# Optimization experiments

Hardware: AMD Instinct MI355X
Metric: run time of the kernel (lower is better)

## Reference

```python
import jax, jax.numpy as jnp
import numpy as np

B, T, H = 4, 2048, 1024
NH, NKV, HD = 16, 4, 64  # heads, kv heads, head_dim

def setup_inputs() -> dict:
    key = jax.random.key(0)
    ks = jax.random.split(key, 5)
    s = 0.02
    return {
        "x": jax.random.normal(ks[0], (B, T, H), dtype=jnp.float32),
        "wq": jax.random.normal(ks[1], (H, NH * HD), dtype=jnp.float32) * s,
        "wk": jax.random.normal(ks[2], (H, NKV * HD), dtype=jnp.float32) * s,
        "wv": jax.random.normal(ks[3], (H, NKV * HD), dtype=jnp.float32) * s,
        "wo": jax.random.normal(ks[4], (NH * HD, H), dtype=jnp.float32) * s,
    }

def reference(x, wq, wk, wv, wo):
    b, t, _ = x.shape
    q = (x @ wq).reshape(b, t, NH, HD).transpose(0, 2, 1, 3)    # [B,NH,T,HD]
    k = (x @ wk).reshape(b, t, NKV, HD).transpose(0, 2, 1, 3)   # [B,NKV,T,HD]
    v = (x @ wv).reshape(b, t, NKV, HD).transpose(0, 2, 1, 3)
    n_rep = NH // NKV
    # repeat_kv: expand each kv head n_rep times along the head axis
    k_rep = jnp.repeat(k, n_rep, axis=1)                        # [B,NH,T,HD]
    v_rep = jnp.repeat(v, n_rep, axis=1)
    scale = 1.0 / np.sqrt(HD).astype(np.float32)
    scores = jnp.einsum('bhqd,bhkd->bhqk', q, k_rep) * scale    # [B,NH,T,T]
    key_pos = jnp.arange(t)[None, :]
    q_pos = jnp.arange(t)[:, None]  # past_len = 0 (no kv cache)
    causal = key_pos > q_pos                                    # [T,T]
    scores = jnp.where(causal[None, None], -jnp.inf, scores)
    probs = jax.nn.softmax(scores, axis=-1)                     # dropout is identity (eval / rate 0)
    attn = jnp.einsum('bhqk,bhkd->bhqd', probs, v_rep)          # [B,NH,T,HD]
    attn = attn.transpose(0, 2, 1, 3).reshape(b, t, NH * HD)
    return attn @ wo
```

## Files before the change

kernel.cpp:

```cpp
#include <hip/hip_runtime.h>
#include <hip/hip_bf16.h>

using bf16 = __hip_bfloat16;
typedef __attribute__((ext_vector_type(8))) short bf16x8;
typedef __attribute__((ext_vector_type(4))) short bf16x4;
typedef __attribute__((ext_vector_type(4))) float f32x4;

typedef const __attribute__((address_space(1))) void* as1_t;
typedef __attribute__((address_space(3))) void* as3_t;
__device__ __forceinline__ void load_lds16(const void* g, void* l) {
    __builtin_amdgcn_global_load_lds((as1_t)g, (as3_t)l, 16, 0, 0);
}

__global__ __launch_bounds__(256) void cast_f32_bf16(const float* __restrict__ src,
                                                     bf16* __restrict__ dst, int n4) {
    int i = (blockIdx.x * 256 + threadIdx.x);
    if (i >= n4) return;
    const float4 v = *(const float4*)(src + (long)i * 4);
    bf16 t[4];
    t[0] = __float2bfloat16(v.x);
    t[1] = __float2bfloat16(v.y);
    t[2] = __float2bfloat16(v.z);
    t[3] = __float2bfloat16(v.w);
    *(uint2*)(dst + (long)i * 4) = *(uint2*)t;
}

__global__ __launch_bounds__(256) void transpose_cast(const float* __restrict__ src,
                                                      int K, int N, bf16* __restrict__ dst) {
    __shared__ float tile[32][33];
    const int tx = threadIdx.x & 31;
    const int ty = threadIdx.x >> 5;
    const int n0 = blockIdx.x * 32;
    const int k0 = blockIdx.y * 32;
    for (int i = 0; i < 32; i += 8)
        tile[ty + i][tx] = src[(long)(k0 + ty + i) * N + n0 + tx];
    __syncthreads();
    for (int i = 0; i < 32; i += 8)
        dst[(long)(n0 + ty + i) * K + k0 + tx] = __float2bfloat16(tile[tx][ty + i]);
}

__global__ __launch_bounds__(256) void transpose_v(const bf16* __restrict__ qkv,
                                                   bf16* __restrict__ vt) {
    __shared__ bf16 tile[64][72];
    const int tb = blockIdx.x, kvh = blockIdx.y, b = blockIdx.z;
    const int r = threadIdx.x >> 3;
    const int c = (threadIdx.x & 7) * 8;
    const bf16* src = qkv + (long)(b * 2048 + tb * 64) * 1536 + 1280 + kvh * 64;
    *(uint4*)&tile[r][c]      = *(const uint4*)(src + (long)r * 1536 + c);
    *(uint4*)&tile[r + 32][c] = *(const uint4*)(src + (long)(r + 32) * 1536 + c);
    __syncthreads();
    bf16* dst = vt + (long)(b * 4 + kvh) * 64 * 2048 + tb * 64;
#pragma unroll
    for (int rr = 0; rr < 2; rr++) {
        const int d = r + rr * 32;
        bf16 t8[8];
#pragma unroll
        for (int e = 0; e < 8; e++) t8[e] = tile[c + e][d];
        *(uint4*)(dst + (long)d * 2048 + c) = *(uint4*)t8;
    }
}

template <bool BF16_OUT>
__global__ __launch_bounds__(256) void gemm_bt(const bf16* __restrict__ A,
                                               const bf16* __restrict__ Bt,
                                               void* __restrict__ C,
                                               int M, int N, int K) {
    __shared__ bf16 Ash[128 * 32];
    __shared__ bf16 Bsh[128 * 32];
    const int tid  = threadIdx.x;
    const int lane = tid & 63;
    const int wid  = tid >> 6;
    const int wm   = (wid >> 1) * 64;
    const int wn   = (wid & 1) * 64;
    const int quad = lane >> 4;
    const int l16  = lane & 15;
    const int bm = blockIdx.x, bn = blockIdx.y;

    const int r_l   = lane >> 2;
    const int cslot = lane & 3;
    const int cdat  = (cslot - (r_l >> 1)) & 3;

    const bf16* pa0 = A  + (long)(bm * 128 + wid * 32 + r_l) * K + cdat * 8;
    const bf16* pa1 = pa0 + (long)16 * K;
    const bf16* pb0 = Bt + (long)(bn * 128 + wid * 32 + r_l) * K + cdat * 8;
    const bf16* pb1 = pb0 + (long)16 * K;
    bf16* la0 = Ash + (wid * 32) * 32;
    bf16* la1 = Ash + (wid * 32 + 16) * 32;
    bf16* lb0 = Bsh + (wid * 32) * 32;
    bf16* lb1 = Bsh + (wid * 32 + 16) * 32;

    const int sw = ((quad + (l16 >> 1)) & 3) * 8;

    f32x4 acc[4][4] = {};

    for (int k0 = 0; k0 < K; k0 += 32) {
        __syncthreads();
        load_lds16(pa0 + k0, la0);
        load_lds16(pa1 + k0, la1);
        load_lds16(pb0 + k0, lb0);
        load_lds16(pb1 + k0, lb1);
        __syncthreads();

        bf16x8 af[4], bfr[4];
#pragma unroll
        for (int i = 0; i < 4; i++) af[i]  = *(const bf16x8*)&Ash[(wm + i * 16 + l16) * 32 + sw];
#pragma unroll
        for (int j = 0; j < 4; j++) bfr[j] = *(const bf16x8*)&Bsh[(wn + j * 16 + l16) * 32 + sw];
#pragma unroll
        for (int i = 0; i < 4; i++)
#pragma unroll
            for (int j = 0; j < 4; j++)
                acc[i][j] = __builtin_amdgcn_mfma_f32_16x16x32_bf16(af[i], bfr[j], acc[i][j], 0, 0, 0);
    }

#pragma unroll
    for (int i = 0; i < 4; i++) {
#pragma unroll
        for (int r = 0; r < 4; r++) {
            const long row = (long)(bm * 128 + wm + i * 16 + quad * 4 + r);
#pragma unroll
            for (int j = 0; j < 4; j++) {
                const int col = bn * 128 + wn + j * 16 + l16;
                const float v = acc[i][j][r];
                if (BF16_OUT) ((bf16*)C)[row * N + col] = __float2bfloat16(v);
                else          ((float*)C)[row * N + col] = v;
            }
        }
    }
}

__global__ __launch_bounds__(256) void attn_kernel(const bf16* __restrict__ qkv,
                                                   const bf16* __restrict__ vt,
                                                   bf16* __restrict__ attn) {
    __shared__ bf16 Ksh[64][72];
    __shared__ bf16 Vsh[64][72];

    const int tid  = threadIdx.x;
    const int lane = tid & 63;
    const int wid  = tid >> 6;
    const int quad = lane >> 4;
    const int l16  = lane & 15;
    const int h    = blockIdx.y;
    const int b    = blockIdx.z;
    const int kvh  = h >> 2;
    const int pb   = blockIdx.x;

    const float ls = 0.125f * 1.44269504f;

    bf16x4 ones;
    { short o1 = (short)0x3F80; short t4[4] = {o1, o1, o1, o1}; ones = *(const bf16x4*)t4; }

    const bf16* kg = qkv + (long)(b * 2048) * 1536 + 1024 + kvh * 64;
    const bf16* vg = vt + (long)(b * 4 + kvh) * 64 * 2048;
    const int r0 = tid >> 3;
    const int c0 = (tid & 7) * 8;

    const bf16* kp0 = kg + (long)r0 * 1536 + c0;
    const bf16* kp1 = kp0 + (long)32 * 1536;
    const bf16* vp0 = vg + (long)r0 * 2048 + c0;
    const bf16* vp1 = vp0 + (long)32 * 2048;

#pragma unroll 1
    for (int seg = 0; seg < 2; ++seg) {
        const int qb     = seg ? pb : (31 - pb);
        const int qblock = qb * 64;
        const int q0     = qblock + wid * 16;

        const bf16* qbase = qkv + (long)(b * 2048 + q0 + l16) * 1536 + h * 64;
        bf16x8 qf[2];
#pragma unroll
        for (int kf = 0; kf < 2; kf++) {
            const bf16* qp = qbase + kf * 32 + quad * 8;
            bf16 t8[8];
#pragma unroll
            for (int e = 0; e < 8; e++) t8[e] = __float2bfloat16(__bfloat162float(qp[e]) * ls);
            qf[kf] = *(const bf16x8*)t8;
        }

        f32x4 o[4] = {};
        f32x4 ol = {};

        uint4 kr0 = *(const uint4*)kp0;
        uint4 kr1 = *(const uint4*)kp1;
        uint4 vr0 = *(const uint4*)vp0;
        uint4 vr1 = *(const uint4*)vp1;

        const int nIter = qb + 1;
        for (int it = 0; it < nIter; ++it) {
            __syncthreads();
            *(uint4*)&Ksh[r0][c0]      = kr0;
            *(uint4*)&Ksh[r0 + 32][c0] = kr1;
            *(uint4*)&Vsh[r0][c0]      = vr0;
            *(uint4*)&Vsh[r0 + 32][c0] = vr1;
            __syncthreads();

            if (it + 1 < nIter) {
                const long ko = (long)(it + 1) * 64 * 1536;
                const long vo = (it + 1) * 64;
                kr0 = *(const uint4*)(kp0 + ko);
                kr1 = *(const uint4*)(kp1 + ko);
                vr0 = *(const uint4*)(vp0 + vo);
                vr1 = *(const uint4*)(vp1 + vo);
            }

            f32x4 s[4] = {};
#pragma unroll
            for (int kvt = 0; kvt < 4; kvt++)
#pragma unroll
                for (int kf = 0; kf < 2; kf++) {
                    const bf16x8 kfr = *(const bf16x8*)&Ksh[kvt * 16 + l16][kf * 32 + quad * 8];
                    s[kvt] = __builtin_amdgcn_mfma_f32_16x16x32_bf16(kfr, qf[kf], s[kvt], 0, 0, 0);
                }

            if (it == nIter - 1) {
                const int qq = wid * 16 + l16;
#pragma unroll
                for (int kvt = 0; kvt < 4; kvt++)
#pragma unroll
                    for (int r = 0; r < 4; r++)
                        if (kvt * 16 + quad * 4 + r > qq) s[kvt][r] = -1e30f;
            }

#pragma unroll
            for (int kvt = 0; kvt < 4; kvt++) {
                float2 p01, p23;
                p01.x = exp2f(s[kvt][0]);
                p01.y = exp2f(s[kvt][1]);
                p23.x = exp2f(s[kvt][2]);
                p23.y = exp2f(s[kvt][3]);
                __hip_bfloat162 pk01 = __float22bfloat162_rn(p01);
                __hip_bfloat162 pk23 = __float22bfloat162_rn(p23);
                bf16x4 pk;
                *(__hip_bfloat162*)&pk       = pk01;
                *((__hip_bfloat162*)&pk + 1) = pk23;

                ol = __builtin_amdgcn_mfma_f32_16x16x16bf16_1k(ones, pk, ol, 0, 0, 0);
#pragma unroll
                for (int dt = 0; dt < 4; dt++) {
                    const bf16x4 vf = *(const bf16x4*)&Vsh[dt * 16 + l16][kvt * 16 + quad * 4];
                    o[dt] = __builtin_amdgcn_mfma_f32_16x16x16bf16_1k(vf, pk, o[dt], 0, 0, 0);
                }
            }
        }

        const float inv = 1.f / ol[0];
        bf16* obase = attn + (long)(b * 2048 + q0 + l16) * 1024 + h * 64;
#pragma unroll
        for (int dt = 0; dt < 4; dt++) {
            bf16 t4[4];
#pragma unroll
            for (int r = 0; r < 4; r++) t4[r] = __float2bfloat16(o[dt][r] * inv);
            *(uint2*)(obase + dt * 16 + quad * 4) = *(uint2*)t4;
        }
    }
}

extern "C" void kernel_launch(void* const* d_in, const int* in_sizes, int n_in,
                              void* d_out, int out_size, void* d_ws, size_t ws_size,
                              hipStream_t stream) {
    const float* x  = (const float*)d_in[0];
    const float* wq = (const float*)d_in[1];
    const float* wk = (const float*)d_in[2];
    const float* wv = (const float*)d_in[3];
    const float* wo = (const float*)d_in[4];
    float* out = (float*)d_out;

    char* ws = (char*)d_ws;
    bf16* xb     = (bf16*)(ws);
    bf16* wqkvT  = (bf16*)(ws + 16777216);
    bf16* woT    = (bf16*)(ws + 19922944);
    bf16* qkv    = (bf16*)(ws + 22020096);
    bf16* vt     = (bf16*)(ws + 47185920);
    bf16* attn   = (bf16*)(ws + 51380224);

    cast_f32_bf16<<<8192, 256, 0, stream>>>(x, xb, 2097152);

    transpose_cast<<<dim3(32, 32), 256, 0, stream>>>(wq, 1024, 1024, wqkvT);
    transpose_cast<<<dim3(8, 32),  256, 0, stream>>>(wk, 1024, 256,  wqkvT + 1024 * 1024);
    transpose_cast<<<dim3(8, 32),  256, 0, stream>>>(wv, 1024, 256,  wqkvT + 1280 * 1024);
    transpose_cast<<<dim3(32, 32), 256, 0, stream>>>(wo, 1024, 1024, woT);

    gemm_bt<true><<<dim3(64, 12), 256, 0, stream>>>(xb, wqkvT, qkv, 8192, 1536, 1024);

    transpose_v<<<dim3(32, 4, 4), 256, 0, stream>>>(qkv, vt);

    attn_kernel<<<dim3(16, 16, 4), 256, 0, stream>>>(qkv, vt, attn);

    gemm_bt<false><<<dim3(64, 8), 256, 0, stream>>>(attn, woT, out, 8192, 1024, 1024);
}
```

Baseline: 236.8 us.

## Deepen GEMM K-tile to 64, swap MFMA operands for vector stores, merge weight transposes

The GEMM now stages a 64-wide K slice per iteration with an 8-chunk XOR-style swizzle. This halves the number of barrier pairs per K loop. MFMA operands are swapped so each lane holds four consecutive output columns, which allows 8-byte bf16 or 16-byte fp32 vector stores in the epilogue instead of scalar stores. The four weight transpose-cast launches are merged into one launch indexed by blockIdx.z, with early exit for the narrower wk/wv blocks. LDS per block doubles, which may lower occupancy.

```diff
diff --git a/kernel.cpp b/kernel.cpp
--- a/kernel.cpp
+++ b/kernel.cpp
@@ -25,8 +25,22 @@
     *(uint2*)(dst + (long)i * 4) = *(uint2*)t;
 }
 
-__global__ __launch_bounds__(256) void transpose_cast(const float* __restrict__ src,
-                                                      int K, int N, bf16* __restrict__ dst) {
+__global__ __launch_bounds__(256) void transpose_all(const float* __restrict__ wq,
+                                                     const float* __restrict__ wk,
+                                                     const float* __restrict__ wv,
+                                                     const float* __restrict__ wo,
+                                                     bf16* __restrict__ wqkvT,
+                                                     bf16* __restrict__ woT) {
+    const int z = blockIdx.z;
+    const float* src;
+    bf16* dst;
+    int N;
+    if (z == 0)      { src = wq; dst = wqkvT;              N = 1024; }
+    else if (z == 1) { src = wo; dst = woT;                N = 1024; }
+    else if (z == 2) { if (blockIdx.x >= 8) return; src = wk; dst = wqkvT + 1024 * 1024; N = 256; }
+    else             { if (blockIdx.x >= 8) return; src = wv; dst = wqkvT + 1280 * 1024; N = 256; }
+    const int K = 1024;
+
     __shared__ float tile[32][33];
     const int tx = threadIdx.x & 31;
     const int ty = threadIdx.x >> 5;
@@ -65,8 +79,8 @@
                                                const bf16* __restrict__ Bt,
                                                void* __restrict__ C,
                                                int M, int N, int K) {
-    __shared__ bf16 Ash[128 * 32];
-    __shared__ bf16 Bsh[128 * 32];
+    __shared__ bf16 Ash[128 * 64];
+    __shared__ bf16 Bsh[128 * 64];
     const int tid  = threadIdx.x;
     const int lane = tid & 63;
     const int wid  = tid >> 6;
@@ -76,54 +90,55 @@
     const int l16  = lane & 15;
     const int bm = blockIdx.x, bn = blockIdx.y;
 
-    const int r_l   = lane >> 2;
-    const int cslot = lane & 3;
-    const int cdat  = (cslot - (r_l >> 1)) & 3;
-
-    const bf16* pa0 = A  + (long)(bm * 128 + wid * 32 + r_l) * K + cdat * 8;
-    const bf16* pa1 = pa0 + (long)16 * K;
-    const bf16* pb0 = Bt + (long)(bn * 128 + wid * 32 + r_l) * K + cdat * 8;
-    const bf16* pb1 = pb0 + (long)16 * K;
-    bf16* la0 = Ash + (wid * 32) * 32;
-    bf16* la1 = Ash + (wid * 32 + 16) * 32;
-    bf16* lb0 = Bsh + (wid * 32) * 32;
-    bf16* lb1 = Bsh + (wid * 32 + 16) * 32;
-
-    const int sw = ((quad + (l16 >> 1)) & 3) * 8;
+    const int r8 = lane >> 3;
+    const int c8 = lane & 7;
+    const int gchunk = (c8 - r8) & 7;
+
+    const bf16* pa = A  + (long)(bm * 128 + wid * 32 + r8) * K + gchunk * 8;
+    const bf16* pb = Bt + (long)(bn * 128 + wid * 32 + r8) * K + gchunk * 8;
+    bf16* lA = Ash + (wid * 32) * 64;
+    bf16* lB = Bsh + (wid * 32) * 64;
 
     f32x4 acc[4][4] = {};
 
-    for (int k0 = 0; k0 < K; k0 += 32) {
+    for (int k0 = 0; k0 < K; k0 += 64) {
         __syncthreads();
-        load_lds16(pa0 + k0, la0);
-        load_lds16(pa1 + k0, la1);
-        load_lds16(pb0 + k0, lb0);
-        load_lds16(pb1 + k0, lb1);
+#pragma unroll
+        for (int j = 0; j < 4; j++) {
+            load_lds16(pa + k0 + (long)(j * 8) * K, lA + j * 8 * 64);
+            load_lds16(pb + k0 + (long)(j * 8) * K, lB + j * 8 * 64);
+        }
         __syncthreads();
 
-        bf16x8 af[4], bfr[4];
-#pragma unroll
-        for (int i = 0; i < 4; i++) af[i]  = *(const bf16x8*)&Ash[(wm + i * 16 + l16) * 32 + sw];
-#pragma unroll
-        for (int j = 0; j < 4; j++) bfr[j] = *(const bf16x8*)&Bsh[(wn + j * 16 + l16) * 32 + sw];
-#pragma unroll
-        for (int i = 0; i < 4; i++)
-#pragma unroll
-            for (int j = 0; j < 4; j++)
-                acc[i][j] = __builtin_amdgcn_mfma_f32_16x16x32_bf16(af[i], bfr[j], acc[i][j], 0, 0, 0);
+#pragma unroll
+        for (int kf = 0; kf < 2; kf++) {
+            const int slot = ((kf * 4 + quad + l16) & 7) * 8;
+            bf16x8 af[4], bfr[4];
+#pragma unroll
+            for (int i = 0; i < 4; i++) af[i]  = *(const bf16x8*)&Ash[(wm + i * 16 + l16) * 64 + slot];
+#pragma unroll
+            for (int j = 0; j < 4; j++) bfr[j] = *(const bf16x8*)&Bsh[(wn + j * 16 + l16) * 64 + slot];
+#pragma unroll
+            for (int i = 0; i < 4; i++)
+#pragma unroll
+                for (int j = 0; j < 4; j++)
+                    acc[i][j] = __builtin_amdgcn_mfma_f32_16x16x32_bf16(bfr[j], af[i], acc[i][j], 0, 0, 0);
+        }
     }
 
 #pragma unroll
     for (int i = 0; i < 4; i++) {
-#pragma unroll
-        for (int r = 0; r < 4; r++) {
-            const long row = (long)(bm * 128 + wm + i * 16 + quad * 4 + r);
-#pragma unroll
-            for (int j = 0; j < 4; j++) {
-                const int col = bn * 128 + wn + j * 16 + l16;
-                const float v = acc[i][j][r];
-                if (BF16_OUT) ((bf16*)C)[row * N + col] = __float2bfloat16(v);
-                else          ((float*)C)[row * N + col] = v;
+        const long m = (long)(bm * 128 + wm + i * 16 + l16);
+#pragma unroll
+        for (int j = 0; j < 4; j++) {
+            const int n = bn * 128 + wn + j * 16 + quad * 4;
+            if (BF16_OUT) {
+                bf16 t4[4];
+#pragma unroll
+                for (int r = 0; r < 4; r++) t4[r] = __float2bfloat16(acc[i][j][r]);
+                *(uint2*)((bf16*)C + m * N + n) = *(uint2*)t4;
+            } else {
+                *(f32x4*)((float*)C + m * N + n) = acc[i][j];
             }
         }
     }
@@ -275,10 +290,7 @@
 
     cast_f32_bf16<<<8192, 256, 0, stream>>>(x, xb, 2097152);
 
-    transpose_cast<<<dim3(32, 32), 256, 0, stream>>>(wq, 1024, 1024, wqkvT);
-    transpose_cast<<<dim3(8, 32),  256, 0, stream>>>(wk, 1024, 256,  wqkvT + 1024 * 1024);
-    transpose_cast<<<dim3(8, 32),  256, 0, stream>>>(wv, 1024, 256,  wqkvT + 1280 * 1024);
-    transpose_cast<<<dim3(32, 32), 256, 0, stream>>>(wo, 1024, 1024, woT);
+    transpose_all<<<dim3(32, 32, 4), 256, 0, stream>>>(wq, wk, wv, wo, wqkvT, woT);
 
     gemm_bt<true><<<dim3(64, 12), 256, 0, stream>>>(xb, wqkvT, qkv, 8192, 1536, 1024);
 
```

Measured after the change: 236.8 us. About the same (+0.0%).
